# Kernel optimization log

Measured on AMD Instinct MI355X. Metric: run time of the kernel, lower is better.

## Reference

```python
import jax, jax.numpy as jnp
import numpy as np

MARGIN = 0.5
EPS = 1e-10


def setup_inputs() -> dict:
    key = jax.random.key(0)
    k1, k2 = jax.random.split(key)
    n, d = 8192, 256
    xs = jax.random.normal(k1, (n, d), dtype=jnp.float32)
    ys = jax.random.randint(k2, (n,), 0, 64, dtype=jnp.int64)
    return {"xs": xs, "ys": ys}


def reference(xs, ys):
    n = xs.shape[0]
    # pairwise squared L2: ||a||^2 + ||b||^2 - 2 a.b  -> [n, n]
    sq = jnp.sum(xs * xs, axis=1)
    dist2 = sq[:, None] + sq[None, :] - 2.0 * (xs @ xs.T)
    dist = jnp.sqrt(jnp.maximum(dist2, EPS))
    # same-label mask (includes diagonal, as in the original)
    mask = (ys[None, :] == ys[:, None]).astype(dist.dtype)  # [n, n]
    pos_cnt = jnp.sum(mask, axis=1)
    neg_cnt = n - pos_cnt
    dist_ap = jnp.sum(dist * mask, axis=1) / pos_cnt
    dist_an = jnp.sum(dist * (1.0 - mask), axis=1) / neg_cnt
    # MarginRankingLoss with y=1: mean(relu(-(dist_an - dist_ap) + margin))
    loss = jnp.mean(jnp.maximum(dist_ap - dist_an + MARGIN, 0.0))
    return loss
```

## Files before the change

kernel.cpp:

```cpp
#include <hip/hip_runtime.h>
#include <math.h>

#define N 8192
#define D 256
#define TILE 128
#define NB (N / TILE)
#define NBLK (NB * (NB + 1) / 2)

typedef _Float16 half8 __attribute__((ext_vector_type(8)));
typedef float f32x4 __attribute__((ext_vector_type(4)));

constexpr float MARGIN = 0.5f;
constexpr float EPS_F  = 1e-10f;


__global__ void prep_kernel(const float* __restrict__ xs,
                            const int* __restrict__ ys_raw,
                            _Float16* __restrict__ x16t, float* __restrict__ sq,
                            int* __restrict__ lbl, float* __restrict__ sums,
                            float* __restrict__ out) {
    const int tid = threadIdx.x;
    const int rb  = blockIdx.x;

    {
        const int r   = tid >> 4;
        const int c16 = tid & 15;
        const int row = rb * 16 + r;

        const float4* src = (const float4*)xs + (size_t)row * (D / 4) + c16 * 4;
        const float4 v0 = src[0], v1 = src[1], v2 = src[2], v3 = src[3];

        half8 h0 = { (_Float16)v0.x, (_Float16)v0.y, (_Float16)v0.z, (_Float16)v0.w,
                     (_Float16)v1.x, (_Float16)v1.y, (_Float16)v1.z, (_Float16)v1.w };
        half8 h1 = { (_Float16)v2.x, (_Float16)v2.y, (_Float16)v2.z, (_Float16)v2.w,
                     (_Float16)v3.x, (_Float16)v3.y, (_Float16)v3.z, (_Float16)v3.w };

        _Float16* dst = x16t + (size_t)rb * 4096 + (c16 * 2) * 128 + r * 8;
        *(half8*)dst         = h0;
        *(half8*)(dst + 128) = h1;

        float s = v0.x*v0.x + v0.y*v0.y + v0.z*v0.z + v0.w*v0.w
                + v1.x*v1.x + v1.y*v1.y + v1.z*v1.z + v1.w*v1.w
                + v2.x*v2.x + v2.y*v2.y + v2.z*v2.z + v2.w*v2.w
                + v3.x*v3.x + v3.y*v3.y + v3.z*v3.z + v3.w*v3.w;
#pragma unroll
        for (int off = 1; off < 16; off <<= 1) s += __shfl_xor(s, off);
        if (c16 == 0) sq[row] = s;
    }

    if (rb < 16) {
        __shared__ int bad_s;
        const int base = rb * 512;
        if (tid == 0) bad_s = 0;
        __syncthreads();
        int bad = 0;
        for (int i = tid; i < 512; i += 256) bad |= (ys_raw[2 * (base + i) + 1] != 0);
        if (bad) atomicOr(&bad_s, 1);
        __syncthreads();
        const bool is64 = (bad_s == 0);
        for (int i = tid; i < 512; i += 256)
            lbl[base + i] = is64 ? ys_raw[2 * (base + i)] : ys_raw[base + i];
    }

    if (rb >= 16 && rb < 48) {
        const int off = (rb - 16) * 512 + tid;
        sums[off]       = 0.f;
        sums[off + 256] = 0.f;
    }
    if (rb == 48 && tid == 0) out[0] = 0.f;
}

__global__ __launch_bounds__(256, 3) void pair_kernel(
    const _Float16* __restrict__ x16t, const int* __restrict__ lbl,
    const float* __restrict__ sq,
    float* __restrict__ sum_same, float* __restrict__ sum_all) {

    const int t = (blockIdx.x % 8) * (NBLK / 8) + blockIdx.x / 8;

    int bj = (int)((sqrtf(8.f * (float)t + 1.f) - 1.f) * 0.5f);
    while ((bj + 1) * (bj + 2) / 2 <= t) ++bj;
    while (bj * (bj + 1) / 2 > t) --bj;
    const int bi    = t - bj * (bj + 1) / 2;
    const bool diag = (bi == bj);
    const int i0 = bi * TILE;
    const int j0 = bj * TILE;

    const int tid  = threadIdx.x;
    const int w    = tid >> 6;
    const int lane = tid & 63;
    const int wm   = w >> 1;
    const int wn   = w & 1;
    const int cl   = lane & 15;
    const int g    = lane >> 4;

    f32x4 acc[4][4];
#pragma unroll
    for (int a = 0; a < 4; ++a)
#pragma unroll
        for (int b = 0; b < 4; ++b) acc[a][b] = (f32x4){0.f, 0.f, 0.f, 0.f};

    const _Float16* pa = x16t + (size_t)((i0 >> 4) + wm * 4) * 4096 + g * 128 + cl * 8;
    const _Float16* pb = x16t + (size_t)((j0 >> 4) + wn * 4) * 4096 + g * 128 + cl * 8;

    half8 af[2][4], bf[2][4];
#pragma unroll
    for (int mf = 0; mf < 4; ++mf) {
        af[0][mf] = *(const half8*)(pa + mf * 4096);
        bf[0][mf] = *(const half8*)(pb + mf * 4096);
    }

#pragma unroll
    for (int t8 = 0; t8 < 8; ++t8) {
        if (t8 < 7) {
            const int koff = (t8 + 1) * 512;
#pragma unroll
            for (int mf = 0; mf < 4; ++mf) {
                af[(t8 + 1) & 1][mf] = *(const half8*)(pa + mf * 4096 + koff);
                bf[(t8 + 1) & 1][mf] = *(const half8*)(pb + mf * 4096 + koff);
            }
        }
#pragma unroll
        for (int mf = 0; mf < 4; ++mf)
#pragma unroll
            for (int nf = 0; nf < 4; ++nf)
                acc[mf][nf] = __builtin_amdgcn_mfma_f32_16x16x32_f16(
                    af[t8 & 1][mf], bf[t8 & 1][nf], acc[mf][nf], 0, 0, 0);
    }

    const int rowbase = i0 + wm * 64;
    const int colbase = j0 + wn * 64;

    float sqj_[4];
    int   yj_[4];
#pragma unroll
    for (int nf = 0; nf < 4; ++nf) {
        const int c = colbase + nf * 16 + cl;
        sqj_[nf] = sq[c];
        yj_[nf]  = lbl[c];
    }

    float cs_all[4], cs_same[4];
#pragma unroll
    for (int nf = 0; nf < 4; ++nf) { cs_all[nf] = 0.f; cs_same[nf] = 0.f; }

#pragma unroll
    for (int b = 0; b < 2; ++b) {
        float rs_all[8], rs_same[8];
#pragma unroll
        for (int e = 0; e < 8; ++e) { rs_all[e] = 0.f; rs_same[e] = 0.f; }

#pragma unroll
        for (int mh = 0; mh < 2; ++mh) {
            const int mf = 2 * b + mh;
#pragma unroll
            for (int r = 0; r < 4; ++r) {
                const int row   = rowbase + mf * 16 + g * 4 + r;
                const float sqi = sq[row];
                const int   yi  = lbl[row];
#pragma unroll
                for (int nf = 0; nf < 4; ++nf) {
                    float d2   = sqi + sqj_[nf] - 2.f * acc[mf][nf][r];
                    float dist = __builtin_amdgcn_sqrtf(fmaxf(d2, EPS_F));
                    if (diag) {
                        const int col = colbase + nf * 16 + cl;
                        if (row == col) dist = 1e-5f;
                    }
                    const float dm = (yi == yj_[nf]) ? dist : 0.f;
                    cs_all[nf] += dist;
                    cs_same[nf] += dm;
                    rs_all[mh * 4 + r] += dist;
                    rs_same[mh * 4 + r] += dm;
                }
            }
        }

        if (!diag) {
#define RSTEP(h, mask, bit)                                                     \
            {                                                                   \
                const bool hi = (cl >> (bit)) & 1;                              \
                _Pragma("unroll")                                               \
                for (int j = 0; j < (h); ++j) {                                 \
                    float sa_ = hi ? rs_all[j] : rs_all[j + (h)];               \
                    float ka_ = hi ? rs_all[j + (h)] : rs_all[j];               \
                    rs_all[j] = ka_ + __shfl_xor(sa_, (mask));                  \
                    float ss_ = hi ? rs_same[j] : rs_same[j + (h)];             \
                    float ks_ = hi ? rs_same[j + (h)] : rs_same[j];             \
                    rs_same[j] = ks_ + __shfl_xor(ss_, (mask));                 \
                }                                                               \
            }
            RSTEP(4, 8, 3)
            RSTEP(2, 4, 2)
            RSTEP(1, 2, 1)
#undef RSTEP
            rs_all[0]  += __shfl_xor(rs_all[0], 1);
            rs_same[0] += __shfl_xor(rs_same[0], 1);

            const int e    = cl >> 1;
            const int rrow = rowbase + (2 * b + (e >> 2)) * 16 + g * 4 + (e & 3);
            if (!(cl & 1)) {
                atomicAdd(&sum_all[rrow],  rs_all[0]);
                atomicAdd(&sum_same[rrow], rs_same[0]);
            }
        }
    }

    {
        const bool hi1 = (g >> 1) & 1;
#pragma unroll
        for (int j = 0; j < 2; ++j) {
            float sa_ = hi1 ? cs_all[j] : cs_all[j + 2];
            float ka_ = hi1 ? cs_all[j + 2] : cs_all[j];
            cs_all[j] = ka_ + __shfl_xor(sa_, 32);
            float ss_ = hi1 ? cs_same[j] : cs_same[j + 2];
            float ks_ = hi1 ? cs_same[j + 2] : cs_same[j];
            cs_same[j] = ks_ + __shfl_xor(ss_, 32);
        }
        const bool hi0 = g & 1;
        {
            float sa_ = hi0 ? cs_all[0] : cs_all[1];
            float ka_ = hi0 ? cs_all[1] : cs_all[0];
            cs_all[0] = ka_ + __shfl_xor(sa_, 16);
            float ss_ = hi0 ? cs_same[0] : cs_same[1];
            float ks_ = hi0 ? cs_same[1] : cs_same[0];
            cs_same[0] = ks_ + __shfl_xor(ss_, 16);
        }
        const int ccol = colbase + g * 16 + cl;
        atomicAdd(&sum_all[ccol],  cs_all[0]);
        atomicAdd(&sum_same[ccol], cs_same[0]);
    }
}

__global__ void finalize_kernel(const float* __restrict__ sum_same,
                                const float* __restrict__ sum_all,
                                const int* __restrict__ lbl,
                                float* __restrict__ out) {
    __shared__ int lh[64];
    __shared__ float wsums[4];
    const int tid  = threadIdx.x;
    const int base = blockIdx.x * 512;
    if (tid < 64) lh[tid] = 0;
    __syncthreads();
    for (int i = tid; i < N; i += 256) atomicAdd(&lh[lbl[i]], 1);
    __syncthreads();

    float local = 0.f;
    for (int i = tid; i < 512; i += 256) {
        const int row  = base + i;
        const float cnt = (float)lh[lbl[row]];
        const float ss  = sum_same[row];
        const float sa  = sum_all[row];
        const float ap  = ss / cnt;
        const float an  = (sa - ss) / ((float)N - cnt);
        local += fmaxf(ap - an + MARGIN, 0.f);
    }
#pragma unroll
    for (int off = 32; off > 0; off >>= 1) local += __shfl_down(local, off);
    const int lane = tid & 63, wave = tid >> 6;
    if (lane == 0) wsums[wave] = local;
    __syncthreads();
    if (tid == 0)
        atomicAdd(out, (wsums[0] + wsums[1] + wsums[2] + wsums[3]) / (float)N);
}

extern "C" void kernel_launch(void* const* d_in, const int* in_sizes, int n_in,
                              void* d_out, int out_size, void* d_ws, size_t ws_size,
                              hipStream_t stream) {
    const float* xs     = (const float*)d_in[0];
    const int*   ys_raw = (const int*)d_in[1];

    float* ws        = (float*)d_ws;
    float* sum_same  = ws;
    float* sum_all   = ws + N;
    float* sqv       = ws + 2 * N;
    int*   lbl       = (int*)(ws + 3 * N);
    _Float16* x16t   = (_Float16*)(ws + 4 * N);

    prep_kernel<<<N / 16, 256, 0, stream>>>(xs, ys_raw, x16t, sqv, lbl,
                                            sum_same, (float*)d_out);

    pair_kernel<<<NBLK, 256, 0, stream>>>(x16t, lbl, sqv, sum_same, sum_all);

    finalize_kernel<<<16, 256, 0, stream>>>(sum_same, sum_all, lbl, (float*)d_out);
}
```

Baseline: 61.53 us.

## Replace global atomics with per-tile partial sums reduced in finalize

The pair kernel no longer does global atomicAdd on the per-row and per-column sums. Each tile combines its two warp halves in shared memory and writes a deterministic partial for each (row block, column block) into a workspace buffer. The finalize kernel then sums the NB partials per row. This removes atomic contention and the zeroing pass, at the cost of extra syncthreads in the pair kernel and a larger finalize read.

```diff
diff --git a/kernel.cpp b/kernel.cpp
--- a/kernel.cpp
+++ b/kernel.cpp
@@ -17,8 +17,7 @@
 __global__ void prep_kernel(const float* __restrict__ xs,
                             const int* __restrict__ ys_raw,
                             _Float16* __restrict__ x16t, float* __restrict__ sq,
-                            int* __restrict__ lbl, float* __restrict__ sums,
-                            float* __restrict__ out) {
+                            int* __restrict__ lbl, float* __restrict__ out) {
     const int tid = threadIdx.x;
     const int rb  = blockIdx.x;
 
@@ -62,18 +61,15 @@
             lbl[base + i] = is64 ? ys_raw[2 * (base + i)] : ys_raw[base + i];
     }
 
-    if (rb >= 16 && rb < 48) {
-        const int off = (rb - 16) * 512 + tid;
-        sums[off]       = 0.f;
-        sums[off + 256] = 0.f;
-    }
     if (rb == 48 && tid == 0) out[0] = 0.f;
 }
 
 __global__ __launch_bounds__(256, 3) void pair_kernel(
     const _Float16* __restrict__ x16t, const int* __restrict__ lbl,
-    const float* __restrict__ sq,
-    float* __restrict__ sum_same, float* __restrict__ sum_all) {
+    const float* __restrict__ sq, float2* __restrict__ part) {
+
+    __shared__ float2 cmb[128];
+    __shared__ float2 rmb[2][2][32];
 
     const int t = (blockIdx.x % 8) * (NBLK / 8) + blockIdx.x / 8;
 
@@ -195,11 +191,17 @@
             rs_all[0]  += __shfl_xor(rs_all[0], 1);
             rs_same[0] += __shfl_xor(rs_same[0], 1);
 
-            const int e    = cl >> 1;
-            const int rrow = rowbase + (2 * b + (e >> 2)) * 16 + g * 4 + (e & 3);
-            if (!(cl & 1)) {
-                atomicAdd(&sum_all[rrow],  rs_all[0]);
-                atomicAdd(&sum_same[rrow], rs_same[0]);
+            const int e     = cl >> 1;
+            const int local = (2 * b + (e >> 2)) * 16 + g * 4 + (e & 3);
+            if (wn == 0) {
+                if (!(cl & 1))
+                    rmb[b][wm][g * 8 + e] = make_float2(rs_all[0], rs_same[0]);
+            }
+            __syncthreads();
+            if (wn == 1 && !(cl & 1)) {
+                const float2 o = rmb[b][wm][g * 8 + e];
+                part[((size_t)bi * NB + bj) * TILE + wm * 64 + local] =
+                    make_float2(o.x + rs_all[0], o.y + rs_same[0]);
             }
         }
     }
@@ -224,35 +226,46 @@
             float ks_ = hi0 ? cs_same[1] : cs_same[0];
             cs_same[0] = ks_ + __shfl_xor(ss_, 16);
         }
-        const int ccol = colbase + g * 16 + cl;
-        atomicAdd(&sum_all[ccol],  cs_all[0]);
-        atomicAdd(&sum_same[ccol], cs_same[0]);
-    }
-}
-
-__global__ void finalize_kernel(const float* __restrict__ sum_same,
-                                const float* __restrict__ sum_all,
+        const int lc = wn * 64 + g * 16 + cl;
+        if (wm == 0) cmb[lc] = make_float2(cs_all[0], cs_same[0]);
+        __syncthreads();
+        if (wm == 1) {
+            const float2 o = cmb[lc];
+            part[((size_t)bj * NB + bi) * TILE + lc] =
+                make_float2(o.x + cs_all[0], o.y + cs_same[0]);
+        }
+    }
+}
+
+__global__ void finalize_kernel(const float2* __restrict__ part,
                                 const int* __restrict__ lbl,
                                 float* __restrict__ out) {
     __shared__ int lh[64];
     __shared__ float wsums[4];
-    const int tid  = threadIdx.x;
-    const int base = blockIdx.x * 512;
+    const int tid = threadIdx.x;
     if (tid < 64) lh[tid] = 0;
     __syncthreads();
     for (int i = tid; i < N; i += 256) atomicAdd(&lh[lbl[i]], 1);
     __syncthreads();
 
-    float local = 0.f;
-    for (int i = tid; i < 512; i += 256) {
-        const int row  = base + i;
-        const float cnt = (float)lh[lbl[row]];
-        const float ss  = sum_same[row];
-        const float sa  = sum_all[row];
-        const float ap  = ss / cnt;
-        const float an  = (sa - ss) / ((float)N - cnt);
-        local += fmaxf(ap - an + MARGIN, 0.f);
-    }
+    const int row = blockIdx.x * 256 + tid;
+    const int p   = row >> 7;
+    const int lr  = row & 127;
+    const float2* base = part + (size_t)p * NB * TILE + lr;
+
+    float sa = 0.f, ss = 0.f;
+#pragma unroll
+    for (int c = 0; c < NB; ++c) {
+        const float2 v = base[(size_t)c * TILE];
+        sa += v.x;
+        ss += v.y;
+    }
+
+    const float cnt = (float)lh[lbl[row]];
+    const float ap  = ss / cnt;
+    const float an  = (sa - ss) / ((float)N - cnt);
+    float local = fmaxf(ap - an + MARGIN, 0.f);
+
 #pragma unroll
     for (int off = 32; off > 0; off >>= 1) local += __shfl_down(local, off);
     const int lane = tid & 63, wave = tid >> 6;
@@ -268,17 +281,16 @@
     const float* xs     = (const float*)d_in[0];
     const int*   ys_raw = (const int*)d_in[1];
 
-    float* ws        = (float*)d_ws;
-    float* sum_same  = ws;
-    float* sum_all   = ws + N;
-    float* sqv       = ws + 2 * N;
-    int*   lbl       = (int*)(ws + 3 * N);
-    _Float16* x16t   = (_Float16*)(ws + 4 * N);
+    float* ws      = (float*)d_ws;
+    float* sqv     = ws;
+    int*   lbl     = (int*)(ws + N);
+    _Float16* x16t = (_Float16*)(ws + 2 * N);
+    float2* part   = (float2*)(ws + 2 * N + N * D / 2);
 
     prep_kernel<<<N / 16, 256, 0, stream>>>(xs, ys_raw, x16t, sqv, lbl,
-                                            sum_same, (float*)d_out);
-
-    pair_kernel<<<NBLK, 256, 0, stream>>>(x16t, lbl, sqv, sum_same, sum_all);
-
-    finalize_kernel<<<16, 256, 0, stream>>>(sum_same, sum_all, lbl, (float*)d_out);
-}
+                                            (float*)d_out);
+
+    pair_kernel<<<NBLK, 256, 0, stream>>>(x16t, lbl, sqv, part);
+
+    finalize_kernel<<<32, 256, 0, stream>>>(part, lbl, (float*)d_out);
+}
```

New measurement: 70.00 us. +13.8%, slower.

## Stage pair-kernel operands through LDS with async global_load_lds triple buffering

Applied to the files above, without the earlier changes.

Changes the fp16 copy of xs from a pre-swizzled fragment layout to plain row-major. The pair kernel now streams A and B tiles into a three-stage LDS ring using global_load_lds, synchronised with explicit vmcnt waits and barriers, and reads MFMA fragments from LDS. Previously each wave loaded its fragments straight from global memory into registers with a two-deep prefetch. The aim is to share tile loads across waves and hide latency more deeply, at the cost of 48KB of LDS, which may reduce occupancy, two barriers per k-step, and possible LDS bank conflicts from the unpadded BK=32 row stride.

```diff
diff --git a/kernel.cpp b/kernel.cpp
--- a/kernel.cpp
+++ b/kernel.cpp
@@ -3,6 +3,7 @@
 
 #define N 8192
 #define D 256
+#define BK 32
 #define TILE 128
 #define NB (N / TILE)
 #define NBLK (NB * (NB + 1) / 2)
@@ -13,10 +14,15 @@
 constexpr float MARGIN = 0.5f;
 constexpr float EPS_F  = 1e-10f;
 
+__device__ inline void load_lds16(const void* g, void* l) {
+    __builtin_amdgcn_global_load_lds(
+        (const __attribute__((address_space(1))) void*)g,
+        (__attribute__((address_space(3))) void*)l, 16, 0, 0);
+}
 
 __global__ void prep_kernel(const float* __restrict__ xs,
                             const int* __restrict__ ys_raw,
-                            _Float16* __restrict__ x16t, float* __restrict__ sq,
+                            _Float16* __restrict__ x16, float* __restrict__ sq,
                             int* __restrict__ lbl, float* __restrict__ sums,
                             float* __restrict__ out) {
     const int tid = threadIdx.x;
@@ -35,9 +41,9 @@
         half8 h1 = { (_Float16)v2.x, (_Float16)v2.y, (_Float16)v2.z, (_Float16)v2.w,
                      (_Float16)v3.x, (_Float16)v3.y, (_Float16)v3.z, (_Float16)v3.w };
 
-        _Float16* dst = x16t + (size_t)rb * 4096 + (c16 * 2) * 128 + r * 8;
-        *(half8*)dst         = h0;
-        *(half8*)(dst + 128) = h1;
+        _Float16* dst = x16 + (size_t)row * D + c16 * 16;
+        *(half8*)dst       = h0;
+        *(half8*)(dst + 8) = h1;
 
         float s = v0.x*v0.x + v0.y*v0.y + v0.z*v0.z + v0.w*v0.w
                 + v1.x*v1.x + v1.y*v1.y + v1.z*v1.z + v1.w*v1.w
@@ -71,9 +77,12 @@
 }
 
 __global__ __launch_bounds__(256, 3) void pair_kernel(
-    const _Float16* __restrict__ x16t, const int* __restrict__ lbl,
+    const _Float16* __restrict__ x16, const int* __restrict__ lbl,
     const float* __restrict__ sq,
     float* __restrict__ sum_same, float* __restrict__ sum_all) {
+
+    __shared__ _Float16 As[3][TILE * BK];
+    __shared__ _Float16 Bs[3][TILE * BK];
 
     const int t = (blockIdx.x % 8) * (NBLK / 8) + blockIdx.x / 8;
 
@@ -99,33 +108,54 @@
 #pragma unroll
         for (int b = 0; b < 4; ++b) acc[a][b] = (f32x4){0.f, 0.f, 0.f, 0.f};
 
-    const _Float16* pa = x16t + (size_t)((i0 >> 4) + wm * 4) * 4096 + g * 128 + cl * 8;
-    const _Float16* pb = x16t + (size_t)((j0 >> 4) + wn * 4) * 4096 + g * 128 + cl * 8;
-
-    half8 af[2][4], bf[2][4];
-#pragma unroll
-    for (int mf = 0; mf < 4; ++mf) {
-        af[0][mf] = *(const half8*)(pa + mf * 4096);
-        bf[0][mf] = *(const half8*)(pb + mf * 4096);
-    }
+    const int c0 = w * 64 + lane;
+    const int r0 = c0 >> 2, kc0 = c0 & 3;
+    const int c1 = 256 + c0;
+    const int r1 = c1 >> 2, kc1 = c1 & 3;
+
+#define STAGE(buf, k0)                                                          \
+    do {                                                                        \
+        load_lds16(x16 + (size_t)(i0 + r0) * D + (k0) + kc0 * 8,                \
+                   &As[buf][(size_t)(w * 64) * 8]);                             \
+        load_lds16(x16 + (size_t)(j0 + r0) * D + (k0) + kc0 * 8,                \
+                   &Bs[buf][(size_t)(w * 64) * 8]);                             \
+        load_lds16(x16 + (size_t)(i0 + r1) * D + (k0) + kc1 * 8,                \
+                   &As[buf][(size_t)(256 + w * 64) * 8]);                       \
+        load_lds16(x16 + (size_t)(j0 + r1) * D + (k0) + kc1 * 8,                \
+                   &Bs[buf][(size_t)(256 + w * 64) * 8]);                       \
+    } while (0)
+
+    STAGE(0, 0);
+    STAGE(1, BK);
 
 #pragma unroll
     for (int t8 = 0; t8 < 8; ++t8) {
-        if (t8 < 7) {
-            const int koff = (t8 + 1) * 512;
-#pragma unroll
-            for (int mf = 0; mf < 4; ++mf) {
-                af[(t8 + 1) & 1][mf] = *(const half8*)(pa + mf * 4096 + koff);
-                bf[(t8 + 1) & 1][mf] = *(const half8*)(pb + mf * 4096 + koff);
-            }
-        }
+        const int cur = t8 % 3;
+        if (t8 < 6) STAGE((t8 + 2) % 3, (t8 + 2) * BK);
+
+        if (t8 < 6)       asm volatile("s_waitcnt vmcnt(8)" ::: "memory");
+        else if (t8 == 6) asm volatile("s_waitcnt vmcnt(4)" ::: "memory");
+        else              asm volatile("s_waitcnt vmcnt(0)" ::: "memory");
+        __builtin_amdgcn_s_barrier();
+
+        half8 af[4], bf[4];
+#pragma unroll
+        for (int mf = 0; mf < 4; ++mf)
+            af[mf] = *(const half8*)&As[cur][(wm * 64 + mf * 16 + cl) * BK + g * 8];
+#pragma unroll
+        for (int nf = 0; nf < 4; ++nf)
+            bf[nf] = *(const half8*)&Bs[cur][(wn * 64 + nf * 16 + cl) * BK + g * 8];
+
 #pragma unroll
         for (int mf = 0; mf < 4; ++mf)
 #pragma unroll
             for (int nf = 0; nf < 4; ++nf)
                 acc[mf][nf] = __builtin_amdgcn_mfma_f32_16x16x32_f16(
-                    af[t8 & 1][mf], bf[t8 & 1][nf], acc[mf][nf], 0, 0, 0);
-    }
+                    af[mf], bf[nf], acc[mf][nf], 0, 0, 0);
+
+        __builtin_amdgcn_s_barrier();
+    }
+#undef STAGE
 
     const int rowbase = i0 + wm * 64;
     const int colbase = j0 + wn * 64;
@@ -268,17 +298,17 @@
     const float* xs     = (const float*)d_in[0];
     const int*   ys_raw = (const int*)d_in[1];
 
-    float* ws        = (float*)d_ws;
-    float* sum_same  = ws;
-    float* sum_all   = ws + N;
-    float* sqv       = ws + 2 * N;
-    int*   lbl       = (int*)(ws + 3 * N);
-    _Float16* x16t   = (_Float16*)(ws + 4 * N);
-
-    prep_kernel<<<N / 16, 256, 0, stream>>>(xs, ys_raw, x16t, sqv, lbl,
+    float* ws       = (float*)d_ws;
+    float* sum_same = ws;
+    float* sum_all  = ws + N;
+    float* sqv      = ws + 2 * N;
+    int*   lbl      = (int*)(ws + 3 * N);
+    _Float16* x16   = (_Float16*)(ws + 4 * N);
+
+    prep_kernel<<<N / 16, 256, 0, stream>>>(xs, ys_raw, x16, sqv, lbl,
                                             sum_same, (float*)d_out);
 
-    pair_kernel<<<NBLK, 256, 0, stream>>>(x16t, lbl, sqv, sum_same, sum_all);
+    pair_kernel<<<NBLK, 256, 0, stream>>>(x16, lbl, sqv, sum_same, sum_all);
 
     finalize_kernel<<<16, 256, 0, stream>>>(sum_same, sum_all, lbl, (float*)d_out);
 }
```

Measured after the change: 58.21 us. 5.4% less time.
